# Kernel tuning notes

Measured on AMD Instinct MI355X. Metric: run time of the kernel, lower is better.

Reference implementation:

```python
import jax, jax.numpy as jnp
import numpy as np

N = 32            # batch (age.shape[0])
N_SAMPLE = 8
S = N * N_SAMPLE  # posterior samples
T = 1024          # len_param
K = 64            # len_window
D = 4             # dim_target
P = 8             # dim_param
LOG2PI = float(np.log(2.0 * np.pi))


def _windows(x, axis, num, size):
    # torch.unfold equivalent, but window axis inserted right after `axis`
    idx = jnp.arange(num)[:, None] + jnp.arange(size)[None, :]
    return jnp.take(x, idx, axis=axis)


def _coeffs(a_pad):
    # a_pad: (2K-2, D, 1) -> AR weight matrix d: (K, K, D)
    # d[t, k] = prod(a[t-K+1+k+1 .. t]) with trailing 1 (reversed cumprod of windows)
    b = _windows(a_pad, 0, K, K - 1)                              # (K, K-1, D, 1)
    c = jnp.flip(jnp.cumprod(jnp.flip(b, 1), axis=1), 1)
    d = jnp.concatenate([c, jnp.ones_like(c[:, :1])], axis=1)      # (K, K, D, 1)
    return d[..., 0]                                               # (K, K, D)


def _window_param(z, d):
    # z: (S, K, D, P); d: (K, K, D) -> param: (S, K, D, P)
    z_pad = jnp.pad(z, ((0, 0), (K - 1, 0), (0, 0), (0, 0)))
    zwin = _windows(z_pad, 1, K, K)                                # (S, K, K, D, P)
    return jnp.einsum('stkdp,tkd->stdp', zwin, d)


def _forward(m, s_raw, a_raw, noise, dim_idx):
    mm = m[:, dim_idx]                         # (T, D, P)
    s = jax.nn.softplus(s_raw[:, dim_idx])     # scale_transform
    a = jax.nn.sigmoid(a_raw[:, dim_idx])      # (T-1, D, 1)
    # ---- first window ----
    a_pad = jnp.pad(a[:K - 1], ((K - 1, 0), (0, 0), (0, 0)))       # (2K-2, D, 1)
    mean = (1.0 - a_pad[K - 2:]) * mm[:K]                          # (K, D, P)
    sw = s[:K]
    z = mean + sw * noise[:, :K]                                   # rsample
    lp = -jnp.log(sw) - 0.5 * LOG2PI - 0.5 * ((z - mean) / sw) ** 2
    param = _window_param(z, _coeffs(a_pad))
    params, lps = [param], [lp]
    # ---- subsequent windows (sequential carry via param[:, -1]) ----
    for l in range(K, T, K):
        r = min(l + K, T)
        aw = a[l - 1:r - 1]                                        # (K, D, 1)
        mean = (1.0 - aw) * mm[l:r]
        sw = s[l:r]
        z = mean + sw * noise[:, l:r]
        lp = -jnp.log(sw) - 0.5 * LOG2PI - 0.5 * ((z - mean) / sw) ** 2
        a_pad = jnp.pad(aw[1:], ((K - 1, 0), (0, 0), (0, 0)))
        p = _window_param(z, _coeffs(a_pad))
        p = p + jnp.cumprod(aw, axis=0)[None] * param[:, -1][:, None]
        params.append(p)
        lps.append(lp)
        param = p
    return jnp.concatenate(params, axis=1), jnp.concatenate(lps, axis=1)


def setup_inputs() -> dict:
    key = jax.random.key(0)
    k = jax.random.split(key, 6)
    return {
        'y': jax.random.normal(k[0], (1, T, D), dtype=jnp.float32),
        'age': jax.random.uniform(k[1], (N,), dtype=jnp.float32),
        'm': 0.1 * jax.random.normal(k[2], (T, D, P), dtype=jnp.float32),
        's_raw': 0.1 * jax.random.normal(k[3], (T, D, P), dtype=jnp.float32) - 6.0,
        'a_raw': jax.random.normal(k[4], (T - 1, D, 1), dtype=jnp.float32),
        'noise': jax.random.normal(k[5], (S, T, D, P), dtype=jnp.float32),
        'cond_sample': jnp.zeros((S, D, P), dtype=jnp.float32),
        'dim_idx': jnp.arange(D, dtype=jnp.int32),
        'compute_log_prob': 1,
    }


def reference(y, age, m, s_raw, a_raw, noise, cond_sample, dim_idx, compute_log_prob):
    param, log_prob = _forward(m, s_raw, a_raw, noise, dim_idx)
    if compute_log_prob:
        return (param, log_prob)
    return param
```

## Files before the change

kernel.cpp:

```cpp
#include <hip/hip_runtime.h>

#define T_DIM 1024
#define D_DIM 4
#define P_DIM 8
#define S_DIM 256
#define DP 32
#define TDP (T_DIM * DP)
#define LOG2PI_F 1.8378770664093453f

typedef float vf4 __attribute__((ext_vector_type(4)));

__global__ __launch_bounds__(1024) void fused_scan(
    const float* __restrict__ noise,
    const float* __restrict__ m,
    const float* __restrict__ s_raw,
    const float* __restrict__ a_raw,
    const int* __restrict__ dim_idx,
    float* __restrict__ param_out,
    float* __restrict__ lp_out)
{
    const int tid = threadIdx.x;
    const int qc  = tid & 7;
    const int cj  = tid >> 3;
    const int cjw = cj & 7;
    const int wg  = tid >> 6;

    const int d  = qc >> 1;
    const int p0 = (qc & 1) * 4;
    const int di = dim_idx[d];

    __shared__ float wtp[16][32];
    __shared__ float wtm8[16][8];
    __shared__ float wci[16][32];

    const size_t sbase = (size_t)blockIdx.x * TDP;
    const int    off0  = cj * 8 * DP + qc * 4;

    vf4   pl[8];
    float Mk[8];
    vf4   rp = (vf4){0.f, 0.f, 0.f, 0.f};
    float rm = 1.0f;
#pragma unroll
    for (int k = 0; k < 8; ++k) {
        const int t = cj * 8 + k;
        const int o = off0 + k * DP;
        const vf4 n  = __builtin_nontemporal_load((const vf4*)(noise + sbase + o));
        const vf4 mv = *(const vf4*)(m     + (t * D_DIM + di) * P_DIM + p0);
        const vf4 sr = *(const vf4*)(s_raw + (t * D_DIM + di) * P_DIM + p0);

        float A = 0.0f;
        if (t > 0) A = 1.0f / (1.0f + __expf(-a_raw[(t - 1) * D_DIM + di]));
        const float oma = 1.0f - A;

        vf4 sv, nl;
        sv.x = __logf(1.0f + __expf(sr.x));  nl.x = -__logf(sv.x) - 0.5f * LOG2PI_F;
        sv.y = __logf(1.0f + __expf(sr.y));  nl.y = -__logf(sv.y) - 0.5f * LOG2PI_F;
        sv.z = __logf(1.0f + __expf(sr.z));  nl.z = -__logf(sv.z) - 0.5f * LOG2PI_F;
        sv.w = __logf(1.0f + __expf(sr.w));  nl.w = -__logf(sv.w) - 0.5f * LOG2PI_F;

        vf4 lp;
        lp.x = nl.x - 0.5f * n.x * n.x;
        lp.y = nl.y - 0.5f * n.y * n.y;
        lp.z = nl.z - 0.5f * n.z * n.z;
        lp.w = nl.w - 0.5f * n.w * n.w;
        __builtin_nontemporal_store(lp, (vf4*)(lp_out + sbase + o));

        vf4 z;
        z.x = oma * mv.x + sv.x * n.x;
        z.y = oma * mv.y + sv.y * n.y;
        z.z = oma * mv.z + sv.z * n.z;
        z.w = oma * mv.w + sv.w * n.w;

        rp.x = z.x + A * rp.x;
        rp.y = z.y + A * rp.y;
        rp.z = z.z + A * rp.z;
        rp.w = z.w + A * rp.w;
        rm  *= A;
        pl[k] = rp;
        Mk[k] = rm;
    }

#pragma unroll
    for (int off = 1; off < 8; off <<= 1) {
        const int dd = off * 8;
        vf4 pp;
        pp.x = __shfl_up(rp.x, dd, 64);
        pp.y = __shfl_up(rp.y, dd, 64);
        pp.z = __shfl_up(rp.z, dd, 64);
        pp.w = __shfl_up(rp.w, dd, 64);
        const float pm = __shfl_up(rm, dd, 64);
        if (cjw >= off) {
            rp.x += rm * pp.x;
            rp.y += rm * pp.y;
            rp.z += rm * pp.z;
            rp.w += rm * pp.w;
            rm *= pm;
        }
    }

    if (cjw == 7) {
        *(vf4*)&wtp[wg][qc * 4] = rp;
        wtm8[wg][qc] = rm;
    }
    __syncthreads();
    if (tid < 32) {
        float c = 0.0f;
#pragma unroll
        for (int g = 0; g < 16; ++g) {
            wci[g][tid] = c;
            c = wtp[g][tid] + wtm8[g][tid >> 2] * c;
        }
    }
    __syncthreads();

    vf4 ep;
    ep.x = __shfl_up(rp.x, 8, 64);
    ep.y = __shfl_up(rp.y, 8, 64);
    ep.z = __shfl_up(rp.z, 8, 64);
    ep.w = __shfl_up(rp.w, 8, 64);
    float em = __shfl_up(rm, 8, 64);
    if (cjw == 0) {
        ep = (vf4){0.f, 0.f, 0.f, 0.f};
        em = 1.0f;
    }
    const vf4 ci = *(const vf4*)&wci[wg][qc * 4];
    vf4 carry;
    carry.x = ep.x + em * ci.x;
    carry.y = ep.y + em * ci.y;
    carry.z = ep.z + em * ci.z;
    carry.w = ep.w + em * ci.w;

#pragma unroll
    for (int k = 0; k < 8; ++k) {
        const int o = off0 + k * DP;
        vf4 pv;
        pv.x = pl[k].x + Mk[k] * carry.x;
        pv.y = pl[k].y + Mk[k] * carry.y;
        pv.z = pl[k].z + Mk[k] * carry.z;
        pv.w = pl[k].w + Mk[k] * carry.w;
        __builtin_nontemporal_store(pv, (vf4*)(param_out + sbase + o));
    }
}

extern "C" void kernel_launch(void* const* d_in, const int* in_sizes, int n_in,
                              void* d_out, int out_size, void* d_ws, size_t ws_size,
                              hipStream_t stream)
{
    const float* m      = (const float*)d_in[2];
    const float* s_raw  = (const float*)d_in[3];
    const float* a_raw  = (const float*)d_in[4];
    const float* noise  = (const float*)d_in[5];
    const int*   dimidx = (const int*)d_in[7];

    float* param_out = (float*)d_out;
    float* lp_out    = param_out + (size_t)S_DIM * TDP;

    fused_scan<<<S_DIM, 1024, 0, stream>>>(noise, m, s_raw, a_raw, dimidx,
                                           param_out, lp_out);
}
```

Baseline: 121.1 us.

## Split each sample across two blocks with float2 lanes and plain stores

Each sample's 32 (d,p) channels are now split across two blocks of 16 channels each, so the grid doubles to 512 blocks and each thread handles float2 instead of float4. The aim is more blocks in flight, to fill the GPU's compute units and improve latency hiding on this memory-bound scan. It also replaces nontemporal stores with ordinary stores, uses a hardware reciprocal for the sigmoid, and adds a minimum-blocks hint to launch_bounds. The trade-off is narrower 8-byte memory accesses per thread and per-block overhead for a duplicated cross-wave scan.

```diff
diff --git a/kernel.cpp b/kernel.cpp
--- a/kernel.cpp
+++ b/kernel.cpp
@@ -8,9 +8,13 @@
 #define TDP (T_DIM * DP)
 #define LOG2PI_F 1.8378770664093453f
 
-typedef float vf4 __attribute__((ext_vector_type(4)));
+typedef float vf2 __attribute__((ext_vector_type(2)));
 
-__global__ __launch_bounds__(1024) void fused_scan(
+__device__ __forceinline__ float sigmoid_fast(float x) {
+    return __builtin_amdgcn_rcpf(1.0f + __expf(-x));
+}
+
+__global__ __launch_bounds__(1024, 8) void fused_scan(
     const float* __restrict__ noise,
     const float* __restrict__ m,
     const float* __restrict__ s_raw,
@@ -20,61 +24,57 @@
     float* __restrict__ lp_out)
 {
     const int tid = threadIdx.x;
-    const int qc  = tid & 7;
+    const int pc  = tid & 7;
     const int cj  = tid >> 3;
     const int cjw = cj & 7;
     const int wg  = tid >> 6;
 
-    const int d  = qc >> 1;
-    const int p0 = (qc & 1) * 4;
+    const int half = blockIdx.x & 1;
+    const int s    = blockIdx.x >> 1;
+
+    const int c0 = half * 16 + pc * 2;
+    const int d  = c0 >> 3;
+    const int p0 = c0 & 7;
     const int di = dim_idx[d];
 
-    __shared__ float wtp[16][32];
+    __shared__ float wtp[16][16];
     __shared__ float wtm8[16][8];
-    __shared__ float wci[16][32];
+    __shared__ float wci[16][16];
 
-    const size_t sbase = (size_t)blockIdx.x * TDP;
-    const int    off0  = cj * 8 * DP + qc * 4;
+    const size_t sbase = (size_t)s * TDP;
+    const int    off0  = cj * 8 * DP + c0;
 
-    vf4   pl[8];
+    vf2   pl[8];
     float Mk[8];
-    vf4   rp = (vf4){0.f, 0.f, 0.f, 0.f};
+    vf2   rp = (vf2){0.f, 0.f};
     float rm = 1.0f;
 #pragma unroll
     for (int k = 0; k < 8; ++k) {
         const int t = cj * 8 + k;
         const int o = off0 + k * DP;
-        const vf4 n  = __builtin_nontemporal_load((const vf4*)(noise + sbase + o));
-        const vf4 mv = *(const vf4*)(m     + (t * D_DIM + di) * P_DIM + p0);
-        const vf4 sr = *(const vf4*)(s_raw + (t * D_DIM + di) * P_DIM + p0);
+        const vf2 n  = __builtin_nontemporal_load((const vf2*)(noise + sbase + o));
+        const vf2 mv = *(const vf2*)(m     + (t * D_DIM + di) * P_DIM + p0);
+        const vf2 sr = *(const vf2*)(s_raw + (t * D_DIM + di) * P_DIM + p0);
 
         float A = 0.0f;
-        if (t > 0) A = 1.0f / (1.0f + __expf(-a_raw[(t - 1) * D_DIM + di]));
+        if (t > 0) A = sigmoid_fast(a_raw[(t - 1) * D_DIM + di]);
         const float oma = 1.0f - A;
 
-        vf4 sv, nl;
+        vf2 sv, nl;
         sv.x = __logf(1.0f + __expf(sr.x));  nl.x = -__logf(sv.x) - 0.5f * LOG2PI_F;
         sv.y = __logf(1.0f + __expf(sr.y));  nl.y = -__logf(sv.y) - 0.5f * LOG2PI_F;
-        sv.z = __logf(1.0f + __expf(sr.z));  nl.z = -__logf(sv.z) - 0.5f * LOG2PI_F;
-        sv.w = __logf(1.0f + __expf(sr.w));  nl.w = -__logf(sv.w) - 0.5f * LOG2PI_F;
 
-        vf4 lp;
+        vf2 lp;
         lp.x = nl.x - 0.5f * n.x * n.x;
         lp.y = nl.y - 0.5f * n.y * n.y;
-        lp.z = nl.z - 0.5f * n.z * n.z;
-        lp.w = nl.w - 0.5f * n.w * n.w;
-        __builtin_nontemporal_store(lp, (vf4*)(lp_out + sbase + o));
+        *(vf2*)(lp_out + sbase + o) = lp;
 
-        vf4 z;
+        vf2 z;
         z.x = oma * mv.x + sv.x * n.x;
         z.y = oma * mv.y + sv.y * n.y;
-        z.z = oma * mv.z + sv.z * n.z;
-        z.w = oma * mv.w + sv.w * n.w;
 
         rp.x = z.x + A * rp.x;
         rp.y = z.y + A * rp.y;
-        rp.z = z.z + A * rp.z;
-        rp.w = z.w + A * rp.w;
         rm  *= A;
         pl[k] = rp;
         Mk[k] = rm;
@@ -83,62 +83,52 @@
 #pragma unroll
     for (int off = 1; off < 8; off <<= 1) {
         const int dd = off * 8;
-        vf4 pp;
+        vf2 pp;
         pp.x = __shfl_up(rp.x, dd, 64);
         pp.y = __shfl_up(rp.y, dd, 64);
-        pp.z = __shfl_up(rp.z, dd, 64);
-        pp.w = __shfl_up(rp.w, dd, 64);
         const float pm = __shfl_up(rm, dd, 64);
         if (cjw >= off) {
             rp.x += rm * pp.x;
             rp.y += rm * pp.y;
-            rp.z += rm * pp.z;
-            rp.w += rm * pp.w;
             rm *= pm;
         }
     }
 
     if (cjw == 7) {
-        *(vf4*)&wtp[wg][qc * 4] = rp;
-        wtm8[wg][qc] = rm;
+        *(vf2*)&wtp[wg][pc * 2] = rp;
+        wtm8[wg][pc] = rm;
     }
     __syncthreads();
-    if (tid < 32) {
+    if (tid < 16) {
         float c = 0.0f;
 #pragma unroll
         for (int g = 0; g < 16; ++g) {
             wci[g][tid] = c;
-            c = wtp[g][tid] + wtm8[g][tid >> 2] * c;
+            c = wtp[g][tid] + wtm8[g][tid >> 1] * c;
         }
     }
     __syncthreads();
 
-    vf4 ep;
+    vf2 ep;
     ep.x = __shfl_up(rp.x, 8, 64);
     ep.y = __shfl_up(rp.y, 8, 64);
-    ep.z = __shfl_up(rp.z, 8, 64);
-    ep.w = __shfl_up(rp.w, 8, 64);
     float em = __shfl_up(rm, 8, 64);
     if (cjw == 0) {
-        ep = (vf4){0.f, 0.f, 0.f, 0.f};
+        ep = (vf2){0.f, 0.f};
         em = 1.0f;
     }
-    const vf4 ci = *(const vf4*)&wci[wg][qc * 4];
-    vf4 carry;
+    const vf2 ci = *(const vf2*)&wci[wg][pc * 2];
+    vf2 carry;
     carry.x = ep.x + em * ci.x;
     carry.y = ep.y + em * ci.y;
-    carry.z = ep.z + em * ci.z;
-    carry.w = ep.w + em * ci.w;
 
 #pragma unroll
     for (int k = 0; k < 8; ++k) {
         const int o = off0 + k * DP;
-        vf4 pv;
+        vf2 pv;
         pv.x = pl[k].x + Mk[k] * carry.x;
         pv.y = pl[k].y + Mk[k] * carry.y;
-        pv.z = pl[k].z + Mk[k] * carry.z;
-        pv.w = pl[k].w + Mk[k] * carry.w;
-        __builtin_nontemporal_store(pv, (vf4*)(param_out + sbase + o));
+        *(vf2*)(param_out + sbase + o) = pv;
     }
 }
 
@@ -155,6 +145,6 @@
     float* param_out = (float*)d_out;
     float* lp_out    = param_out + (size_t)S_DIM * TDP;
 
-    fused_scan<<<S_DIM, 1024, 0, stream>>>(noise, m, s_raw, a_raw, dimidx,
-                                           param_out, lp_out);
+    fused_scan<<<S_DIM * 2, 1024, 0, stream>>>(noise, m, s_raw, a_raw, dimidx,
+                                               param_out, lp_out);
 }
```

Result: slower. 131.8 us (+8.8%).
